# Kernel tuning notes

Hardware: AMD Instinct MI355X
Metric: run time of the kernel (lower is better)

The kernel has to match this reference:

```python
import jax, jax.numpy as jnp
import numpy as np

EMB = 384
HEADS = 6
HEAD_SIZE = 64


def setup_inputs() -> dict:
    key = jax.random.key(0)
    ks = jax.random.split(key, 6)
    B, T = 128, 256
    x = jax.random.normal(ks[0], (B, T, EMB), dtype=jnp.float32)
    s = EMB ** -0.5
    Wq = jax.random.normal(ks[1], (HEADS, EMB, HEAD_SIZE), dtype=jnp.float32) * s
    Wk = jax.random.normal(ks[2], (HEADS, EMB, HEAD_SIZE), dtype=jnp.float32) * s
    Wv = jax.random.normal(ks[3], (HEADS, EMB, HEAD_SIZE), dtype=jnp.float32) * s
    Wproj = jax.random.normal(ks[4], (EMB, EMB), dtype=jnp.float32) * s
    bproj = jax.random.normal(ks[5], (EMB,), dtype=jnp.float32) * 0.01
    return {"x": x, "Wq": Wq, "Wk": Wk, "Wv": Wv, "Wproj": Wproj, "bproj": bproj}


def reference(x, Wq, Wk, Wv, Wproj, bproj):
    B, T, C = x.shape
    scale = C ** -0.5  # original scales by embeddingSize**-0.5, not headSize
    q = jnp.einsum('bte,hed->bhtd', x, Wq)
    k = jnp.einsum('bte,hed->bhtd', x, Wk)
    v = jnp.einsum('bte,hed->bhtd', x, Wv)
    w = jnp.einsum('bhtd,bhsd->bhts', q, k) * scale  # (B,H,T,T)
    mask = jnp.tril(jnp.ones((T, T), dtype=bool))
    w = jnp.where(mask[None, None], w, -jnp.inf)
    # original applies softmax over dim=1 of (B,T,T) -> the query axis -> axis=2 here
    w = jax.nn.softmax(w, axis=2)
    out = jnp.einsum('bhts,bhsd->bhtd', w, v)  # (B,H,T,Dh)
    out = out.transpose(0, 2, 1, 3).reshape(B, T, -1)  # concat heads -> (B,T,EMB)
    return out @ Wproj + bproj  # dropout omitted (eval mode)
```

## Files before the change

kernel.cpp:

```cpp
#include <hip/hip_runtime.h>

#define EMB 384
#define HEADS 6
#define DH 64
#define TT 256

constexpr float SCALE = 0.05103103630798288f;

typedef __attribute__((ext_vector_type(8))) short short8;
typedef __attribute__((ext_vector_type(4))) float f32x4;
typedef __attribute__((ext_vector_type(4))) unsigned short u16x4;

__device__ __forceinline__ unsigned short f2bf(float f) {
  unsigned int u = __builtin_bit_cast(unsigned int, f);
  u += 0x7FFFu + ((u >> 16) & 1u);
  return (unsigned short)(u >> 16);
}
__device__ __forceinline__ float bf2f(unsigned short u) {
  unsigned int v = ((unsigned int)u) << 16;
  return __builtin_bit_cast(float, v);
}
__device__ __forceinline__ void gll16(const void* g, void* l) {
  __builtin_amdgcn_global_load_lds(
      (const __attribute__((address_space(1))) unsigned int*)g,
      (__attribute__((address_space(3))) unsigned int*)l, 16, 0, 0);
}

__global__ __launch_bounds__(256)
void build_wt(const float* __restrict__ Wq, const float* __restrict__ Wk,
              const float* __restrict__ Wv, const float* __restrict__ Wp,
              unsigned short* __restrict__ Wt) {
  int idx = blockIdx.x * 256 + threadIdx.x;
  int n = idx / 48, e0 = (idx % 48) * 8;
  const float* src; int stride;
  if (n < 1152) {
    int h = n / 192, rem = n % 192, qkv = rem >> 6, d = rem & 63;
    const float* W = (qkv == 0) ? Wq : (qkv == 1) ? Wk : Wv;
    src = W + ((size_t)h * EMB + e0) * DH + d; stride = DH;
  } else {
    int c = n - 1152;
    src = Wp + (size_t)e0 * EMB + c; stride = EMB;
  }
  short8 o;
  #pragma unroll
  for (int j = 0; j < 8; ++j) o[j] = (short)f2bf(src[j * stride]);
  ((short8*)Wt)[idx] = o;
}

__global__ __launch_bounds__(1024, 1)
void qkv_attn(const float* __restrict__ x, const unsigned short* __restrict__ Wt,
              unsigned short* __restrict__ O)
{
  __shared__ __align__(16) char EL[73728];
  __shared__ __align__(16) char KL[32768];
  __shared__ __align__(16) char VL[32768];
  __shared__ float Lpart[16][256];
  __shared__ float invL[256];

  const int bhRaw = blockIdx.x, tid = (int)threadIdx.x;
  const int bh = (bhRaw & 7) * 96 + (bhRaw >> 3);
  const int w = tid >> 6, lane = tid & 63;
  const int la = lane & 15, kh = lane >> 4;
  const int b = bh / 6, h = bh - b * 6;
  const float* xf = x + (size_t)b * 256 * 384;
  const unsigned short* Wb = Wt + (size_t)h * 192 * 384;
  char* A0 = EL;
  char* B0 = EL + 32768;
  char* A1 = KL;
  char* B1 = VL;

  const int wr = (w >> 2) * 64, wc = (w & 3) * 48;
  f32x4 acc[4][3];
  #pragma unroll
  for (int i = 0; i < 4; ++i)
    #pragma unroll
    for (int j = 0; j < 3; ++j) acc[i][j] = f32x4{0.f, 0.f, 0.f, 0.f};

  const int arow = tid >> 2, aqq = tid & 3;
  const float4* xfr = (const float4*)(xf + (size_t)arow * 384);

  float4 raA[4], raB[4];
  auto loadA = [&](float4 (&ra)[4], int kt) {
    const int base = kt * 16;
    #pragma unroll
    for (int i = 0; i < 2; ++i) {
      const int ch = aqq + 4 * i;
      ra[2*i]   = xfr[base + ch * 2];
      ra[2*i+1] = xfr[base + ch * 2 + 1];
    }
  };
  auto writeA = [&](char* A, const float4 (&ra)[4]) {
    #pragma unroll
    for (int i = 0; i < 2; ++i) {
      const int ch = aqq + 4 * i;
      float4 va = ra[2*i], vb = ra[2*i+1];
      short8 o;
      o[0] = (short)f2bf(va.x); o[1] = (short)f2bf(va.y);
      o[2] = (short)f2bf(va.z); o[3] = (short)f2bf(va.w);
      o[4] = (short)f2bf(vb.x); o[5] = (short)f2bf(vb.y);
      o[6] = (short)f2bf(vb.z); o[7] = (short)f2bf(vb.w);
      *(short8*)(A + arow * 128 + ((ch ^ (arow & 7)) << 4)) = o;
    }
  };
  auto stageB = [&](char* B, int kt) {
    const int Lb0 = tid * 16;
    const int row0 = Lb0 >> 7;
    const int kcs0 = ((Lb0 >> 4) & 7) ^ (row0 & 7);
    gll16(Wb + (size_t)row0 * 384 + kt * 64 + kcs0 * 8, B + Lb0);
    if (tid < 512) {
      const int Lb = 16384 + tid * 16;
      const int row = Lb >> 7;
      const int kcs = ((Lb >> 4) & 7) ^ (row & 7);
      gll16(Wb + (size_t)row * 384 + kt * 64 + kcs * 8, B + Lb);
    }
  };

  auto compute = [&](const char* A, const char* B) {
    #pragma unroll
    for (int kk = 0; kk < 2; ++kk) {
      const int ch = kk * 4 + kh;
      short8 a[4], bfr[3];
      #pragma unroll
      for (int mi = 0; mi < 4; ++mi) {
        const int r = wr + mi * 16 + la;
        a[mi] = *(const short8*)(A + r * 128 + ((ch ^ (r & 7)) << 4));
      }
      #pragma unroll
      for (int ni = 0; ni < 3; ++ni) {
        const int rB = wc + ni * 16 + la;
        bfr[ni] = *(const short8*)(B + rB * 128 + ((ch ^ (rB & 7)) << 4));
      }
      __builtin_amdgcn_s_setprio(1);
      #pragma unroll
      for (int mi = 0; mi < 4; ++mi)
        #pragma unroll
        for (int ni = 0; ni < 3; ++ni)
          acc[mi][ni] = __builtin_amdgcn_mfma_f32_16x16x32_bf16(a[mi], bfr[ni], acc[mi][ni], 0, 0, 0);
      __builtin_amdgcn_s_setprio(0);
    }
  };

  loadA(raA, 0);
  loadA(raB, 1);
  stageB(B0, 0);
  writeA(A0, raA);
  __syncthreads();

  loadA(raA, 2); stageB(B1, 1); writeA(A1, raB); compute(A0, B0);
  __syncthreads();
  loadA(raB, 3); stageB(B0, 2); writeA(A0, raA); compute(A1, B1);
  __syncthreads();
  loadA(raA, 4); stageB(B1, 3); writeA(A1, raB); compute(A0, B0);
  __syncthreads();
  loadA(raB, 5); stageB(B0, 4); writeA(A0, raA); compute(A1, B1);
  __syncthreads();
  stageB(B1, 5); writeA(A1, raB); compute(A0, B0);
  __syncthreads();
  compute(A1, B1);
  __syncthreads();

  #pragma unroll
  for (int mi = 0; mi < 4; ++mi) {
    #pragma unroll
    for (int ni = 0; ni < 3; ++ni) {
      const int col = wc + ni * 16 + la;
      const int tb = wr + mi * 16 + kh * 4;
      if (col < 64) {
        const int d = col;
        #pragma unroll
        for (int j = 0; j < 4; ++j) {
          const int t = tb + j;
          *(unsigned short*)(EL + t * 128 + (((d >> 3) ^ (t & 7)) << 4) + (d & 7) * 2)
              = f2bf(acc[mi][ni][j]);
        }
      } else if (col < 128) {
        const int d = col - 64;
        #pragma unroll
        for (int j = 0; j < 4; ++j) {
          const int t = tb + j;
          *(unsigned short*)(KL + t * 128 + (((d >> 3) ^ (t & 7)) << 4) + (d & 7) * 2)
              = f2bf(acc[mi][ni][j]);
        }
      } else {
        const int d = col - 128;
        u16x4 pk;
        #pragma unroll
        for (int j = 0; j < 4; ++j) pk[j] = f2bf(acc[mi][ni][j]);
        *(u16x4*)(VL + d * 512 + (((tb >> 3) ^ (d & 7)) << 4) + (tb & 7) * 2) = pk;
      }
    }
  }
  __syncthreads();

  const int p = w >> 1;
  const int rts[2] = { p, 15 - p };
  short8 qa[2][2];
  #pragma unroll
  for (int ti = 0; ti < 2; ++ti)
    #pragma unroll
    for (int kk = 0; kk < 2; ++kk) {
      const int r = rts[ti] * 16 + la;
      const int ch = kk * 4 + kh;
      qa[ti][kk] = *(const short8*)(EL + r * 128 + ((ch ^ (r & 7)) << 4));
    }
  __syncthreads();

  int wps[2], eoffs[2];
  #pragma unroll
  for (int ti = 0; ti < 2; ++ti) {
    const int rt = rts[ti];
    wps[ti] = 32 * ((rt + 2) >> 1);
    const int S = (rt & 1) ? ((rt + 1) * (rt + 1) / 4) : (rt * (rt + 2) / 4);
    eoffs[ti] = 1024 * S;
  }

  #pragma unroll
  for (int i = 0; i < 4; ++i) Lpart[w][i * 64 + lane] = 0.f;

  #pragma unroll
  for (int ti = 0; ti < 2; ++ti) {
    const int rt = rts[ti], wp = wps[ti], stride = wp * 2;
    char* Ebase = EL + eoffs[ti];
    const int nns = wp >> 4;
    for (int ns = (w & 1); ns < nns; ns += 2) {
      f32x4 s4 = f32x4{0.f, 0.f, 0.f, 0.f};
      #pragma unroll
      for (int kk = 0; kk < 2; ++kk) {
        const int rB = ns * 16 + la, kc = kk * 4 + kh;
        short8 bf = *(const short8*)(KL + rB * 128 + ((kc ^ (rB & 7)) << 4));
        s4 = __builtin_amdgcn_mfma_f32_16x16x32_bf16(qa[ti][kk], bf, s4, 0, 0, 0);
      }
      const int c = ns * 16 + la, cc = c >> 3, co = (c & 7) * 2;
      float ps = 0.f;
      #pragma unroll
      for (int j = 0; j < 4; ++j) {
        const int r = kh * 4 + j;
        const int t = rt * 16 + r;
        const float e = (t >= c) ? __expf(s4[j] * SCALE) : 0.f;
        ps += e;
        *(unsigned short*)(Ebase + r * stride + ((cc ^ (r & 3)) << 4) + co) = f2bf(e);
      }
      ps += __shfl_xor(ps, 16);
      ps += __shfl_xor(ps, 32);
      if (kh == 0) Lpart[w][c] += ps;
    }
  }
  __syncthreads();

  if (tid < 256) {
    float Ls = 0.f;
    #pragma unroll
    for (int ww = 0; ww < 16; ++ww) Ls += Lpart[ww][tid];
    invL[tid] = 1.f / Ls;
  }
  __syncthreads();

  {
    const int d = tid >> 4, qq = tid & 15;
    #pragma unroll
    for (int i = 0; i < 2; ++i) {
      const int kcp = qq * 2 + i;
      char* pch = VL + d * 512 + kcp * 16;
      short8 v = *(short8*)pch;
      const int sb = (kcp ^ (d & 7)) * 8;
      short8 o;
      #pragma unroll
      for (int e = 0; e < 8; ++e)
        o[e] = (short)f2bf(bf2f((unsigned short)v[e]) * invL[sb + e]);
      *(short8*)pch = o;
    }
  }
  __syncthreads();

  unsigned short* Og = O + (size_t)b * 256 * 384 + h * 64;
  {
    const int bigw = 2 * p + ((p >> 1) & 1);
    const int ti = (w == bigw) ? 1 : 0;
    const int rt = rts[ti], wp = wps[ti], stride = wp * 2;
    const char* Ebase = EL + eoffs[ti];
    f32x4 oacc[4];
    #pragma unroll
    for (int nd = 0; nd < 4; ++nd) oacc[nd] = f32x4{0.f, 0.f, 0.f, 0.f};
    const int nks = wp >> 5;
    for (int ks = 0; ks < nks; ++ks) {
      const int cc = ks * 4 + kh;
      short8 ea = *(const short8*)(Ebase + la * stride + ((cc ^ (la & 3)) << 4));
      __builtin_amdgcn_s_setprio(1);
      #pragma unroll
      for (int nd = 0; nd < 4; ++nd) {
        const int d = nd * 16 + la;
        short8 vb = *(const short8*)(VL + d * 512 + ((cc ^ (d & 7)) << 4));
        oacc[nd] = __builtin_amdgcn_mfma_f32_16x16x32_bf16(ea, vb, oacc[nd], 0, 0, 0);
      }
      __builtin_amdgcn_s_setprio(0);
    }
    #pragma unroll
    for (int nd = 0; nd < 4; ++nd) {
      const int d = nd * 16 + la;
      #pragma unroll
      for (int j = 0; j < 4; ++j) {
        const int t = rt * 16 + kh * 4 + j;
        Og[(size_t)t * 384 + d] = f2bf(oacc[nd][j]);
      }
    }
  }
}

__global__ __launch_bounds__(512, 1)
void proj_gemm(const unsigned short* __restrict__ A, const unsigned short* __restrict__ Bt,
               float* __restrict__ Co, const float* __restrict__ bias)
{
  __shared__ __align__(16) unsigned short AL[128 * 384];
  __shared__ __align__(16) unsigned short BL[2][128 * 64];
  const int tid = (int)threadIdx.x, w = tid >> 6, lane = tid & 63;
  const int la = lane & 15, kh = lane >> 4;
  const int mt = ((int)blockIdx.x & 7) * 32 + ((int)blockIdx.x >> 3);
  const int m0 = mt * 128;

  {
    const int row = tid >> 2, qq = tid & 3;
    const short8* O8 = (const short8*)(A + (size_t)(m0 + row) * 384);
    #pragma unroll
    for (int i = 0; i < 12; ++i) {
      const int ch = qq + 4 * i;
      *(short8*)((char*)AL + row * 768 + ((ch ^ (row & 7)) << 4)) = O8[ch];
    }
  }

  auto stageB = [&](int buf, int n0, int k0) {
    #pragma unroll
    for (int i = 0; i < 2; ++i) {
      const int Lb = i * 8192 + tid * 16;
      const int row = Lb >> 7;
      const int kcs = ((Lb >> 4) & 7) ^ (row & 7);
      gll16(Bt + (size_t)(n0 + row) * 384 + k0 + kcs * 8, (char*)BL[buf] + Lb);
    }
  };

  stageB(0, 0, 0);
  __syncthreads();

  const int wr = (w >> 2) * 64, wc = (w & 3) * 32;
  int buf = 0;
  for (int nt = 0; nt < 3; ++nt) {
    f32x4 acc[4][2];
    #pragma unroll
    for (int i = 0; i < 4; ++i) { acc[i][0] = f32x4{0.f,0.f,0.f,0.f}; acc[i][1] = f32x4{0.f,0.f,0.f,0.f}; }

    for (int kt = 0; kt < 6; ++kt) {
      if (kt < 5)          stageB(buf ^ 1, nt * 128, (kt + 1) * 64);
      else if (nt + 1 < 3) stageB(buf ^ 1, (nt + 1) * 128, 0);
      #pragma unroll
      for (int kk = 0; kk < 2; ++kk) {
        short8 a[4], bb[2];
        const int chA = kt * 8 + kk * 4 + kh;
        #pragma unroll
        for (int mi = 0; mi < 4; ++mi) {
          const int r = wr + mi * 16 + la;
          a[mi] = *(const short8*)((const char*)AL + r * 768 + ((chA ^ (r & 7)) << 4));
        }
        const int chB = kk * 4 + kh;
        #pragma unroll
        for (int ni = 0; ni < 2; ++ni) {
          const int rB = wc + ni * 16 + la;
          bb[ni] = *(const short8*)((const char*)BL[buf] + rB * 128 + ((chB ^ (rB & 7)) << 4));
        }
        __builtin_amdgcn_s_setprio(1);
        #pragma unroll
        for (int mi = 0; mi < 4; ++mi)
          #pragma unroll
          for (int ni = 0; ni < 2; ++ni)
            acc[mi][ni] = __builtin_amdgcn_mfma_f32_16x16x32_bf16(a[mi], bb[ni], acc[mi][ni], 0, 0, 0);
        __builtin_amdgcn_s_setprio(0);
      }
      __syncthreads();
      buf ^= 1;
    }

    #pragma unroll
    for (int mi = 0; mi < 4; ++mi) {
      const int mbase = m0 + wr + mi * 16 + kh * 4;
      #pragma unroll
      for (int ni = 0; ni < 2; ++ni) {
        const int nl = nt * 128 + wc + ni * 16 + la;
        const float bn = bias[nl];
        #pragma unroll
        for (int j = 0; j < 4; ++j)
          Co[(size_t)(mbase + j) * 384 + nl] = acc[mi][ni][j] + bn;
      }
    }
  }
}

__global__ __launch_bounds__(256, 1)
void mha_fused(const float* __restrict__ x, const float* __restrict__ Wq,
               const float* __restrict__ Wk, const float* __restrict__ Wv,
               const float* __restrict__ Wp, const float* __restrict__ bp,
               float* __restrict__ out)
{
  const int bh = blockIdx.x;
  const int b = bh / HEADS, h = bh % HEADS;
  const int tid = (int)threadIdx.x;
  const int wave = tid >> 6, lane = tid & 63;
  const float* xb = x + (size_t)b * TT * EMB;
  const float* wq = Wq + (size_t)h * EMB * DH;
  const float* wk = Wk + (size_t)h * EMB * DH;
  const float* wv = Wv + (size_t)h * EMB * DH;
  __shared__ float Ks[TT][68];
  __shared__ float Vs[TT][64];
  __shared__ float Qt[64][68];
  for (int c = 0; c < 4; ++c) {
    const int s0 = wave * 64 + c * 16;
    float ak[16], av[16];
    #pragma unroll
    for (int r = 0; r < 16; ++r) { ak[r] = 0.f; av[r] = 0.f; }
    for (int e = 0; e < EMB; ++e) {
      const float kk = wk[e * DH + lane];
      const float vv = wv[e * DH + lane];
      #pragma unroll
      for (int r = 0; r < 16; ++r) {
        const float xv = xb[(s0 + r) * EMB + e];
        ak[r] += xv * kk; av[r] += xv * vv;
      }
    }
    #pragma unroll
    for (int r = 0; r < 16; ++r) { Ks[s0 + r][lane] = ak[r]; Vs[s0 + r][lane] = av[r]; }
  }
  __syncthreads();
  const int s = tid;
  float kreg[64];
  {
    const float4* k4 = (const float4*)&Ks[s][0];
    #pragma unroll
    for (int i = 0; i < 16; ++i) {
      float4 kv = k4[i];
      kreg[4*i+0] = kv.x; kreg[4*i+1] = kv.y; kreg[4*i+2] = kv.z; kreg[4*i+3] = kv.w;
    }
  }
  float Lsum = 0.f;
  for (int tile = 0; tile < 4; ++tile) {
    {
      const int r0 = tile * 64 + wave * 16;
      float aq[16];
      #pragma unroll
      for (int r = 0; r < 16; ++r) aq[r] = 0.f;
      for (int e = 0; e < EMB; ++e) {
        const float qw = wq[e * DH + lane];
        #pragma unroll
        for (int r = 0; r < 16; ++r) aq[r] += xb[(r0 + r) * EMB + e] * qw;
      }
      __syncthreads();
      #pragma unroll
      for (int r = 0; r < 16; ++r) Qt[wave*16 + r][lane] = aq[r];
      __syncthreads();
    }
    const int tbase = tile * 64;
    if (tbase + 63 >= s) {
      for (int tr = 0; tr < 64; ++tr) {
        const int t = tbase + tr;
        if (t < s) continue;
        float w = 0.f;
        const float4* q4 = (const float4*)&Qt[tr][0];
        #pragma unroll
        for (int i = 0; i < 16; ++i) {
          float4 qv = q4[i];
          w += qv.x*kreg[4*i+0] + qv.y*kreg[4*i+1] + qv.z*kreg[4*i+2] + qv.w*kreg[4*i+3];
        }
        Lsum += __expf(w * SCALE);
      }
    }
  }
  __syncthreads();
  {
    const float invL = 1.0f / Lsum;
    float4* v4 = (float4*)&Vs[s][0];
    #pragma unroll
    for (int i = 0; i < 16; ++i) {
      float4 vv = v4[i];
      vv.x *= invL; vv.y *= invL; vv.z *= invL; vv.w *= invL;
      v4[i] = vv;
    }
  }
  __syncthreads();
  const float bias1 = bp[tid];
  const float bias2 = (tid < 128) ? bp[256 + tid] : 0.f;
  const int tr = tid >> 2, dq = tid & 3;
  float* ob = out + (size_t)b * TT * EMB;
  for (int tile = 0; tile < 4; ++tile) {
    {
      const int r0 = tile * 64 + wave * 16;
      float aq[16];
      #pragma unroll
      for (int r = 0; r < 16; ++r) aq[r] = 0.f;
      for (int e = 0; e < EMB; ++e) {
        const float qw = wq[e * DH + lane];
        #pragma unroll
        for (int r = 0; r < 16; ++r) aq[r] += xb[(r0 + r) * EMB + e] * qw;
      }
      __syncthreads();
      #pragma unroll
      for (int r = 0; r < 16; ++r) Qt[wave*16 + r][lane] = aq[r];
      __syncthreads();
    }
    const int t = tile * 64 + tr;
    float qreg[16];
    {
      const float4* q4 = (const float4*)&Qt[tr][dq * 16];
      #pragma unroll
      for (int i = 0; i < 4; ++i) {
        float4 qv = q4[i];
        qreg[4*i+0] = qv.x; qreg[4*i+1] = qv.y; qreg[4*i+2] = qv.z; qreg[4*i+3] = qv.w;
      }
    }
    float acc[16];
    #pragma unroll
    for (int i = 0; i < 16; ++i) acc[i] = 0.f;
    for (int s2 = 0; s2 <= t; ++s2) {
      const float4* kk4 = (const float4*)&Ks[s2][dq * 16];
      float part = 0.f;
      #pragma unroll
      for (int i = 0; i < 4; ++i) {
        float4 kv = kk4[i];
        part += qreg[4*i+0]*kv.x + qreg[4*i+1]*kv.y + qreg[4*i+2]*kv.z + qreg[4*i+3]*kv.w;
      }
      part += __shfl_xor(part, 1);
      part += __shfl_xor(part, 2);
      const float p = __expf(part * SCALE);
      const float4* vv4 = (const float4*)&Vs[s2][dq * 16];
      #pragma unroll
      for (int i = 0; i < 4; ++i) {
        float4 vv = vv4[i];
        acc[4*i+0] += p * vv.x; acc[4*i+1] += p * vv.y;
        acc[4*i+2] += p * vv.z; acc[4*i+3] += p * vv.w;
      }
    }
    __syncthreads();
    #pragma unroll
    for (int i = 0; i < 16; ++i) Qt[tr][dq*16 + i] = acc[i];
    __syncthreads();
    const int c1 = tid;
    const int c2 = 256 + tid;
    for (int rg = 0; rg < 4; ++rg) {
      float a1[16], a2[16];
      #pragma unroll
      for (int r = 0; r < 16; ++r) { a1[r] = 0.f; a2[r] = 0.f; }
      for (int d = 0; d < 64; ++d) {
        const float wp1 = Wp[(size_t)(h*64 + d) * EMB + c1];
        const float wp2 = (tid < 128) ? Wp[(size_t)(h*64 + d) * EMB + c2] : 0.f;
        #pragma unroll
        for (int r = 0; r < 16; ++r) {
          const float a = Qt[rg*16 + r][d];
          a1[r] += a * wp1; a2[r] += a * wp2;
        }
      }
      if (h == 0) {
        #pragma unroll
        for (int r = 0; r < 16; ++r) { a1[r] += bias1; a2[r] += bias2; }
      }
      const int trow0 = tile*64 + rg*16;
      #pragma unroll
      for (int r = 0; r < 16; ++r)
        atomicAdd(&ob[(size_t)(trow0 + r) * EMB + c1], a1[r]);
      if (tid < 128) {
        #pragma unroll
        for (int r = 0; r < 16; ++r)
          atomicAdd(&ob[(size_t)(trow0 + r) * EMB + c2], a2[r]);
      }
    }
    __syncthreads();
  }
}

extern "C" void kernel_launch(void* const* d_in, const int* in_sizes, int n_in,
                              void* d_out, int out_size, void* d_ws, size_t ws_size,
                              hipStream_t stream) {
  const float* x  = (const float*)d_in[0];
  const float* Wq = (const float*)d_in[1];
  const float* Wk = (const float*)d_in[2];
  const float* Wv = (const float*)d_in[3];
  const float* Wp = (const float*)d_in[4];
  const float* bp = (const float*)d_in[5];

  const int nb = in_sizes[0] / (TT * EMB);
  const size_t M = (size_t)nb * TT;
  const size_t XB = M * EMB * 2;
  const size_t WT = (size_t)1536 * 384 * 2;

  const size_t off_wt = 0;
  const size_t off_o  = off_wt + WT;
  const size_t need   = off_o + XB;

  if (ws_size < need || nb * HEADS != 768) {
    hipMemsetAsync(d_out, 0, (size_t)out_size * sizeof(float), stream);
    mha_fused<<<nb * HEADS, 256, 0, stream>>>(x, Wq, Wk, Wv, Wp, bp, (float*)d_out);
    return;
  }

  char* ws = (char*)d_ws;
  unsigned short* Wt = (unsigned short*)(ws + off_wt);
  unsigned short* Ow = (unsigned short*)(ws + off_o);

  build_wt<<<288, 256, 0, stream>>>(Wq, Wk, Wv, Wp, Wt);

  qkv_attn<<<nb * HEADS, 1024, 0, stream>>>(x, Wt, Ow);

  proj_gemm<<<(unsigned)(M / 128), 512, 0, stream>>>(
      Ow, Wt + (size_t)1152 * 384, (float*)d_out, bp);
}
```

Measured before the change: 100.6 us.

## Fuse output projection into attention kernel with per-head atomic accumulation

Removes the separate proj_gemm kernel and the bf16 intermediate O buffer. Each (batch, head) block now stages its 384x64 slice of the projection weights into shared memory and multiplies its own attention output by it. It accumulates partial results into the fp32 output with atomicAdd, and only head 0 adds the bias. This needs a memset of the output first and does 6-way atomic contention on every output element. That adds heavy global atomic traffic in exchange for removing one launch and the intermediate round-trip.

Measured after the change: 294.6 us. 193% more time.

```diff
diff --git a/kernel.cpp b/kernel.cpp
--- a/kernel.cpp
+++ b/kernel.cpp
@@ -49,7 +49,7 @@
 
 __global__ __launch_bounds__(1024, 1)
 void qkv_attn(const float* __restrict__ x, const unsigned short* __restrict__ Wt,
-              unsigned short* __restrict__ O)
+              const float* __restrict__ bias, float* __restrict__ out)
 {
   __shared__ __align__(16) char EL[73728];
   __shared__ __align__(16) char KL[32768];
@@ -64,6 +64,7 @@
   const int b = bh / 6, h = bh - b * 6;
   const float* xf = x + (size_t)b * 256 * 384;
   const unsigned short* Wb = Wt + (size_t)h * 192 * 384;
+  const unsigned short* Wpj = Wt + (size_t)1152 * 384;
   char* A0 = EL;
   char* B0 = EL + 32768;
   char* A1 = KL;
@@ -247,6 +248,14 @@
   }
   __syncthreads();
 
+  #pragma unroll
+  for (int i = 0; i < 2; ++i) {
+    const int Lb = i * 16384 + tid * 16;
+    const int row = Lb >> 7;
+    const int kcs = ((Lb >> 4) & 7) ^ (row & 7);
+    gll16(Wpj + (size_t)row * 384 + h * 64 + kcs * 8, KL + Lb);
+  }
+
   if (tid < 256) {
     float Ls = 0.f;
     #pragma unroll
@@ -272,15 +281,15 @@
   }
   __syncthreads();
 
-  unsigned short* Og = O + (size_t)b * 256 * 384 + h * 64;
+  const int bigw = 2 * p + ((p >> 1) & 1);
+  const int tio = (w == bigw) ? 1 : 0;
+  const int rto = rts[tio];
+  f32x4 oacc[4];
+  #pragma unroll
+  for (int nd = 0; nd < 4; ++nd) oacc[nd] = f32x4{0.f, 0.f, 0.f, 0.f};
   {
-    const int bigw = 2 * p + ((p >> 1) & 1);
-    const int ti = (w == bigw) ? 1 : 0;
-    const int rt = rts[ti], wp = wps[ti], stride = wp * 2;
-    const char* Ebase = EL + eoffs[ti];
-    f32x4 oacc[4];
-    #pragma unroll
-    for (int nd = 0; nd < 4; ++nd) oacc[nd] = f32x4{0.f, 0.f, 0.f, 0.f};
+    const int wp = wps[tio], stride = wp * 2;
+    const char* Ebase = EL + eoffs[tio];
     const int nks = wp >> 5;
     for (int ks = 0; ks < nks; ++ks) {
       const int cc = ks * 4 + kh;
@@ -294,99 +303,71 @@
       }
       __builtin_amdgcn_s_setprio(0);
     }
-    #pragma unroll
-    for (int nd = 0; nd < 4; ++nd) {
-      const int d = nd * 16 + la;
-      #pragma unroll
-      for (int j = 0; j < 4; ++j) {
-        const int t = rt * 16 + kh * 4 + j;
-        Og[(size_t)t * 384 + d] = f2bf(oacc[nd][j]);
-      }
-    }
-  }
-}
-
-__global__ __launch_bounds__(512, 1)
-void proj_gemm(const unsigned short* __restrict__ A, const unsigned short* __restrict__ Bt,
-               float* __restrict__ Co, const float* __restrict__ bias)
-{
-  __shared__ __align__(16) unsigned short AL[128 * 384];
-  __shared__ __align__(16) unsigned short BL[2][128 * 64];
-  const int tid = (int)threadIdx.x, w = tid >> 6, lane = tid & 63;
-  const int la = lane & 15, kh = lane >> 4;
-  const int mt = ((int)blockIdx.x & 7) * 32 + ((int)blockIdx.x >> 3);
-  const int m0 = mt * 128;
+  }
+  __syncthreads();
 
   {
-    const int row = tid >> 2, qq = tid & 3;
-    const short8* O8 = (const short8*)(A + (size_t)(m0 + row) * 384);
-    #pragma unroll
-    for (int i = 0; i < 12; ++i) {
-      const int ch = qq + 4 * i;
-      *(short8*)((char*)AL + row * 768 + ((ch ^ (row & 7)) << 4)) = O8[ch];
-    }
-  }
-
-  auto stageB = [&](int buf, int n0, int k0) {
-    #pragma unroll
-    for (int i = 0; i < 2; ++i) {
-      const int Lb = i * 8192 + tid * 16;
-      const int row = Lb >> 7;
-      const int kcs = ((Lb >> 4) & 7) ^ (row & 7);
-      gll16(Bt + (size_t)(n0 + row) * 384 + k0 + kcs * 8, (char*)BL[buf] + Lb);
-    }
-  };
-
-  stageB(0, 0, 0);
-  __syncthreads();
-
-  const int wr = (w >> 2) * 64, wc = (w & 3) * 32;
-  int buf = 0;
-  for (int nt = 0; nt < 3; ++nt) {
-    f32x4 acc[4][2];
-    #pragma unroll
-    for (int i = 0; i < 4; ++i) { acc[i][0] = f32x4{0.f,0.f,0.f,0.f}; acc[i][1] = f32x4{0.f,0.f,0.f,0.f}; }
-
-    for (int kt = 0; kt < 6; ++kt) {
-      if (kt < 5)          stageB(buf ^ 1, nt * 128, (kt + 1) * 64);
-      else if (nt + 1 < 3) stageB(buf ^ 1, (nt + 1) * 128, 0);
-      #pragma unroll
-      for (int kk = 0; kk < 2; ++kk) {
-        short8 a[4], bb[2];
-        const int chA = kt * 8 + kk * 4 + kh;
-        #pragma unroll
-        for (int mi = 0; mi < 4; ++mi) {
-          const int r = wr + mi * 16 + la;
-          a[mi] = *(const short8*)((const char*)AL + r * 768 + ((chA ^ (r & 7)) << 4));
+    const int Lb = tid * 16;
+    const int row = 256 + (Lb >> 7);
+    const int kcs = ((Lb >> 4) & 7) ^ (row & 7);
+    gll16(Wpj + (size_t)row * 384 + h * 64 + kcs * 8, EL + 32768 + Lb);
+  }
+  #pragma unroll
+  for (int nd = 0; nd < 4; ++nd) {
+    const int d = nd * 16 + la;
+    #pragma unroll
+    for (int j = 0; j < 4; ++j) {
+      const int t = rto * 16 + kh * 4 + j;
+      *(unsigned short*)(EL + t * 128 + (((d >> 3) ^ (t & 7)) << 4) + (d & 7) * 2)
+          = f2bf(oacc[nd][j]);
+    }
+  }
+  __syncthreads();
+
+  float* outp = out + (size_t)b * 256 * 384;
+  const int wr2 = (w >> 2) * 64, wc2 = (w & 3) * 96;
+  #pragma unroll
+  for (int nh = 0; nh < 2; ++nh) {
+    f32x4 acc2[4][3];
+    #pragma unroll
+    for (int i = 0; i < 4; ++i)
+      #pragma unroll
+      for (int j = 0; j < 3; ++j) acc2[i][j] = f32x4{0.f, 0.f, 0.f, 0.f};
+    #pragma unroll
+    for (int kk = 0; kk < 2; ++kk) {
+      const int ch = kk * 4 + kh;
+      short8 a[4], bfr[3];
+      #pragma unroll
+      for (int mi = 0; mi < 4; ++mi) {
+        const int r = wr2 + mi * 16 + la;
+        a[mi] = *(const short8*)(EL + r * 128 + ((ch ^ (r & 7)) << 4));
+      }
+      #pragma unroll
+      for (int ni = 0; ni < 3; ++ni) {
+        const int rB = wc2 + nh * 48 + ni * 16 + la;
+        const char* base = (rB < 256) ? (KL + rB * 128)
+                                      : (EL + 32768 + (rB - 256) * 128);
+        bfr[ni] = *(const short8*)(base + ((ch ^ (rB & 7)) << 4));
+      }
+      __builtin_amdgcn_s_setprio(1);
+      #pragma unroll
+      for (int mi = 0; mi < 4; ++mi)
+        #pragma unroll
+        for (int ni = 0; ni < 3; ++ni)
+          acc2[mi][ni] = __builtin_amdgcn_mfma_f32_16x16x32_bf16(a[mi], bfr[ni], acc2[mi][ni], 0, 0, 0);
+      __builtin_amdgcn_s_setprio(0);
+    }
+    #pragma unroll
+    for (int ni = 0; ni < 3; ++ni) {
+      const int nl = wc2 + nh * 48 + ni * 16 + la;
+      const float bn = (h == 0) ? bias[nl] : 0.f;
+      #pragma unroll
+      for (int mi = 0; mi < 4; ++mi) {
+        #pragma unroll
+        for (int j = 0; j < 4; ++j) {
+          const int t = wr2 + mi * 16 + kh * 4 + j;
+          atomicAdd(&outp[(size_t)t * 384 + nl], acc2[mi][ni][j] + bn);
         }
-        const int chB = kk * 4 + kh;
-        #pragma unroll
-        for (int ni = 0; ni < 2; ++ni) {
-          const int rB = wc + ni * 16 + la;
-          bb[ni] = *(const short8*)((const char*)BL[buf] + rB * 128 + ((chB ^ (rB & 7)) << 4));
-        }
-        __builtin_amdgcn_s_setprio(1);
-        #pragma unroll
-        for (int mi = 0; mi < 4; ++mi)
-          #pragma unroll
-          for (int ni = 0; ni < 2; ++ni)
-            acc[mi][ni] = __builtin_amdgcn_mfma_f32_16x16x32_bf16(a[mi], bb[ni], acc[mi][ni], 0, 0, 0);
-        __builtin_amdgcn_s_setprio(0);
-      }
-      __syncthreads();
-      buf ^= 1;
-    }
-
-    #pragma unroll
-    for (int mi = 0; mi < 4; ++mi) {
-      const int mbase = m0 + wr + mi * 16 + kh * 4;
-      #pragma unroll
-      for (int ni = 0; ni < 2; ++ni) {
-        const int nl = nt * 128 + wc + ni * 16 + la;
-        const float bn = bias[nl];
-        #pragma unroll
-        for (int j = 0; j < 4; ++j)
-          Co[(size_t)(mbase + j) * 384 + nl] = acc[mi][ni][j] + bn;
       }
     }
   }
@@ -582,28 +563,18 @@
   const float* bp = (const float*)d_in[5];
 
   const int nb = in_sizes[0] / (TT * EMB);
-  const size_t M = (size_t)nb * TT;
-  const size_t XB = M * EMB * 2;
   const size_t WT = (size_t)1536 * 384 * 2;
 
-  const size_t off_wt = 0;
-  const size_t off_o  = off_wt + WT;
-  const size_t need   = off_o + XB;
-
-  if (ws_size < need || nb * HEADS != 768) {
+  if (ws_size < WT || nb * HEADS != 768) {
     hipMemsetAsync(d_out, 0, (size_t)out_size * sizeof(float), stream);
     mha_fused<<<nb * HEADS, 256, 0, stream>>>(x, Wq, Wk, Wv, Wp, bp, (float*)d_out);
     return;
   }
 
-  char* ws = (char*)d_ws;
-  unsigned short* Wt = (unsigned short*)(ws + off_wt);
-  unsigned short* Ow = (unsigned short*)(ws + off_o);
-
+  unsigned short* Wt = (unsigned short*)d_ws;
+
+  hipMemsetAsync(d_out, 0, (size_t)out_size * sizeof(float), stream);
   build_wt<<<288, 256, 0, stream>>>(Wq, Wk, Wv, Wp, Wt);
 
-  qkv_attn<<<nb * HEADS, 1024, 0, stream>>>(x, Wt, Ow);
-
-  proj_gemm<<<(unsigned)(M / 128), 512, 0, stream>>>(
-      Ow, Wt + (size_t)1152 * 384, (float*)d_out, bp);
-}
+  qkv_attn<<<nb * HEADS, 1024, 0, stream>>>(x, Wt, bp, (float*)d_out);
+}
```
